# Kernel tuning notes

Measured on AMD Instinct MI355X. Metric: run time of the kernel, lower is better.

## Reference

```python
import jax, jax.numpy as jnp
import numpy as np

N, E, D, H = 100000, 200000, 384, 768
BN_EPS = 1e-5


def setup_inputs() -> dict:
    key = jax.random.key(0)
    ks = jax.random.split(key, 8)
    w = lambda k, sh: jax.random.normal(k, sh, jnp.float32) * 0.02
    return {
        "x": jax.random.normal(ks[0], (N, D), jnp.float32),
        "edge_attr": jax.random.normal(ks[1], (E, D), jnp.float32),
        "gamma": jnp.ones((D,), jnp.float32),
        "beta": jnp.zeros((D,), jnp.float32),
        "eps": jnp.zeros((), jnp.float32),          # GINE train_eps, init 0
        "W_edge": w(ks[2], (D, D)),
        "b_edge": jnp.zeros((D,), jnp.float32),
        "W1": w(ks[3], (D, H)),
        "b1": jnp.zeros((H,), jnp.float32),
        "W2": w(ks[4], (H, D)),
        "b2": jnp.zeros((D,), jnp.float32),
        "edge_index": jax.random.randint(ks[5], (2, E), 0, N, jnp.int32),
    }


def reference(x, edge_attr, gamma, beta, eps, W_edge, b_edge, W1, b1, W2, b2, edge_index):
    # BatchNorm1d over the node (batch) dimension, training statistics
    mu = jnp.mean(x, axis=0)
    var = jnp.var(x, axis=0)
    h = (x - mu) * jax.lax.rsqrt(var + BN_EPS) * gamma + beta  # [N, D]

    src, dst = edge_index[0], edge_index[1]  # j -> i (PyG source_to_target)
    # GINEConv message: relu(x_j + lin(edge_attr))
    msg = jax.nn.relu(h[src] + edge_attr @ W_edge + b_edge)     # [E, D]
    agg = jax.ops.segment_sum(msg, dst, num_segments=N)         # sum aggregation

    # nn((1+eps)*x_i + agg) where nn = Linear->GELU->Linear
    z = (1.0 + eps) * h + agg
    z = jax.nn.gelu(z @ W1 + b1, approximate=False) @ W2 + b2

    # residual + outer GELU activation (drop_path/dropout = identity at eval)
    return x + jax.nn.gelu(z, approximate=False)
```

## Files before the change

### kernel.cpp

```cpp
#include <hip/hip_runtime.h>
#include <hip/hip_bf16.h>

#define Df 384
#define Hf 768
#define SCAN_CH 4096

typedef __bf16 bf16x8 __attribute__((ext_vector_type(8)));
typedef float f32x4 __attribute__((ext_vector_type(4)));

struct __attribute__((aligned(4))) U12 { unsigned int x, y, z; };

__device__ inline unsigned short f2bf(float f) {
    __hip_bfloat16 h = __float2bfloat16(f);
    return __builtin_bit_cast(unsigned short, h);
}
__device__ inline float bf2f(unsigned short u) {
    unsigned int v = ((unsigned int)u) << 16;
    return __builtin_bit_cast(float, v);
}
__device__ inline float lobf(unsigned int v) { return bf2f((unsigned short)(v & 0xffff)); }
__device__ inline float hibf(unsigned int v) { return bf2f((unsigned short)(v >> 16)); }
__device__ inline unsigned int pk2(float a, float b) {
    return (unsigned int)f2bf(a) | ((unsigned int)f2bf(b) << 16);
}
__device__ inline float gelu_(float v) {
    return 0.5f * v * (1.0f + erff(v * 0.70710678118654752f));
}
__device__ inline void gload16(const void* g, void* l) {
    __builtin_amdgcn_global_load_lds(
        (const __attribute__((address_space(1))) unsigned int*)g,
        (__attribute__((address_space(3))) unsigned int*)l, 16, 0, 0);
}

__global__ void bn_stats(const float* __restrict__ x, float* __restrict__ stats, int N) {
    int t = threadIdx.x;
    int c4 = (t % 96) * 4;
    int rs = t / 96;
    float s0 = 0, s1 = 0, s2 = 0, s3 = 0, q0 = 0, q1 = 0, q2 = 0, q3 = 0;
    for (int r = blockIdx.x * 2 + rs; r < N; r += gridDim.x * 2) {
        float4 v = *(const float4*)(x + (size_t)r * Df + c4);
        s0 += v.x; s1 += v.y; s2 += v.z; s3 += v.w;
        q0 += v.x * v.x; q1 += v.y * v.y; q2 += v.z * v.z; q3 += v.w * v.w;
    }
    unsafeAtomicAdd(&stats[c4 + 0], s0);
    unsafeAtomicAdd(&stats[c4 + 1], s1);
    unsafeAtomicAdd(&stats[c4 + 2], s2);
    unsafeAtomicAdd(&stats[c4 + 3], s3);
    unsafeAtomicAdd(&stats[Df + c4 + 0], q0);
    unsafeAtomicAdd(&stats[Df + c4 + 1], q1);
    unsafeAtomicAdd(&stats[Df + c4 + 2], q2);
    unsafeAtomicAdd(&stats[Df + c4 + 3], q3);
}

__global__ void bn_finalize(const float* __restrict__ stats,
                            const float* __restrict__ gamma,
                            const float* __restrict__ beta,
                            float* __restrict__ coef, int N) {
    int c = threadIdx.x;
    float invN = 1.0f / (float)N;
    float mu = stats[c] * invN;
    float var = stats[Df + c] * invN - mu * mu;
    float rs = rsqrtf(var + 1e-5f);
    float a = gamma[c] * rs;
    coef[c] = a;
    coef[Df + c] = beta[c] - mu * a;
}

__global__ void h_kernel(const float* __restrict__ x, const float* __restrict__ coef,
                         unsigned short* __restrict__ hb, int tot8) {
    int i = blockIdx.x * 256 + threadIdx.x;
    if (i >= tot8) return;
    size_t base = (size_t)i * 8;
    int c = (int)(base % Df);
    float4 x0 = *(const float4*)(x + base);
    float4 x1 = *(const float4*)(x + base + 4);
    const float* a = coef + c;
    const float* b = coef + Df + c;
    uint4 o;
    o.x = pk2(x0.x * a[0] + b[0], x0.y * a[1] + b[1]);
    o.y = pk2(x0.z * a[2] + b[2], x0.w * a[3] + b[3]);
    o.z = pk2(x1.x * a[4] + b[4], x1.y * a[5] + b[5]);
    o.w = pk2(x1.z * a[6] + b[6], x1.w * a[7] + b[7]);
    *(uint4*)(hb + base) = o;
}

__global__ void wtrans3(const float* __restrict__ We, const float* __restrict__ W1,
                        const float* __restrict__ W2,
                        unsigned short* __restrict__ WeT, unsigned short* __restrict__ W1T,
                        unsigned short* __restrict__ W2T) {
    int idx = blockIdx.x * 256 + threadIdx.x;
    if (idx < Df * Df) {
        int k = idx / Df, n = idx % Df;
        WeT[n * Df + k] = f2bf(We[idx]);
    } else if (idx < Df * Df + Df * Hf) {
        int i = idx - Df * Df;
        int k = i / Hf, n = i % Hf;
        W1T[(size_t)n * Df + k] = f2bf(W1[i]);
    } else if (idx < Df * Df + 2 * Df * Hf) {
        int i = idx - (Df * Df + Df * Hf);
        int k = i / Df, n = i % Df;
        W2T[(size_t)n * Hf + k] = f2bf(W2[i]);
    }
}

__global__ void degree_k(const int* __restrict__ dst, int* __restrict__ deg, int E) {
    int e = blockIdx.x * 256 + threadIdx.x;
    if (e < E) atomicAdd(&deg[dst[e]], 1);
}

__global__ void scan1(const int* __restrict__ deg, int* __restrict__ off,
                      int* __restrict__ sums, int N) {
    __shared__ int ts[256];
    int t = threadIdx.x;
    int base = blockIdx.x * SCAN_CH + t * 16;
    int v[16];
    int s = 0;
    for (int j = 0; j < 16; j++) {
        int idx = base + j;
        int d = (idx < N) ? deg[idx] : 0;
        v[j] = s;
        s += d;
    }
    ts[t] = s;
    __syncthreads();
    for (int o = 1; o < 256; o <<= 1) {
        int add = (t >= o) ? ts[t - o] : 0;
        __syncthreads();
        ts[t] += add;
        __syncthreads();
    }
    int pre = t ? ts[t - 1] : 0;
    for (int j = 0; j < 16; j++) {
        int idx = base + j;
        if (idx < N) off[idx] = pre + v[j];
    }
    if (t == 255) sums[blockIdx.x] = ts[255];
}

__global__ void scan2(int* __restrict__ sums, int nb) {
    int acc = 0;
    for (int b = 0; b < nb; b++) { int v = sums[b]; sums[b] = acc; acc += v; }
    sums[nb] = acc;
}

__global__ void scan3(int* __restrict__ off, const int* __restrict__ sums, int N, int nb) {
    int idx = blockIdx.x * 256 + threadIdx.x;
    if (idx < N) off[idx] += sums[idx / SCAN_CH];
    else if (idx == N) off[N] = sums[nb];
}

__global__ void fill_k(const int* __restrict__ dst, const int* __restrict__ src,
                       int* __restrict__ cursor, int* __restrict__ srcp,
                       int* __restrict__ pose, int E) {
    int e = blockIdx.x * 256 + threadIdx.x;
    if (e >= E) return;
    int pos = atomicAdd(&cursor[dst[e]], 1);
    srcp[pos] = src[e];
    pose[e] = pos;
}

__global__ __launch_bounds__(256) void aggregate(
    const unsigned short* __restrict__ msgl, const unsigned short* __restrict__ hb,
    const int* __restrict__ off, const int* __restrict__ srcp,
    const float* __restrict__ epsp,
    unsigned short* __restrict__ zb, int N) {
    int lane = threadIdx.x & 63;
    int wid = threadIdx.x >> 6;
    int nwaves = gridDim.x * 4;
    float s1p = 1.0f + epsp[0];
    int loff = lane * 6;
    for (int i = blockIdx.x * 4 + wid; i < N; i += nwaves) {
        int o0 = off[i], o1 = off[i + 1];
        float a0 = 0, a1 = 0, a2 = 0, a3 = 0, a4 = 0, a5 = 0;
        for (int p = o0; p < o1; ++p) {
            int s = srcp[p];
            U12 mv = *(const U12*)(msgl + (size_t)p * Df + loff);
            U12 hv = *(const U12*)(hb + (size_t)s * Df + loff);
            a0 += fmaxf(lobf(mv.x) + lobf(hv.x), 0.f);
            a1 += fmaxf(hibf(mv.x) + hibf(hv.x), 0.f);
            a2 += fmaxf(lobf(mv.y) + lobf(hv.y), 0.f);
            a3 += fmaxf(hibf(mv.y) + hibf(hv.y), 0.f);
            a4 += fmaxf(lobf(mv.z) + lobf(hv.z), 0.f);
            a5 += fmaxf(hibf(mv.z) + hibf(hv.z), 0.f);
        }
        U12 hv = *(const U12*)(hb + (size_t)i * Df + loff);
        U12 o;
        o.x = pk2(s1p * lobf(hv.x) + a0, s1p * hibf(hv.x) + a1);
        o.y = pk2(s1p * lobf(hv.y) + a2, s1p * hibf(hv.y) + a3);
        o.z = pk2(s1p * lobf(hv.z) + a4, s1p * hibf(hv.z) + a5);
        *(U12*)(zb + (size_t)i * Df + loff) = o;
    }
}

template <int KTOT, int EPI>
__global__ __launch_bounds__(256, 3) void gemm_strip(
    const unsigned short* __restrict__ Ab, const unsigned short* __restrict__ Bt,
    const float* __restrict__ bias,
    unsigned short* __restrict__ outb, const float* __restrict__ xres,
    float* __restrict__ outf, int M, int ncols, int ldo) {
    constexpr int NKT = KTOT / 32;
    constexpr int NH = KTOT / 384;
    __shared__ __align__(16) unsigned short Bs[64 * 48 * 8];

    const int t = threadIdx.x;
    const int nwg = gridDim.x;
    const int orig = blockIdx.x;
    const int xcd = orig & 7;
    const int q = nwg >> 3, r = nwg & 7;
    const int wgid = (xcd < r ? xcd * (q + 1) : r * (q + 1) + (xcd - r) * q) + (orig >> 3);
    const int strip = wgid / ncols;
    const int cb = (wgid - strip * ncols) * 64;

    const int lane = t & 63;
    const int wid = t >> 6;
    const int fr = lane & 15;
    const int kg = lane >> 4;

    auto stageB = [&](int koff) {
#pragma unroll
        for (int s_ = 0; s_ < 12; s_++) {
            int u = s_ * 256 + t;
            int col = u / 48;
            int pos = u - col * 48;
            gload16(Bt + (size_t)(cb + col) * KTOT + koff + ((pos ^ (col & 7)) << 3),
                    &Bs[(s_ * 256 + wid * 64) * 8]);
        }
    };

    int ra0 = strip * 128 + wid * 32 + fr;      if (ra0 >= M) ra0 = M - 1;
    int ra1 = strip * 128 + wid * 32 + 16 + fr; if (ra1 >= M) ra1 = M - 1;
    const unsigned short* pA0 = Ab + (size_t)ra0 * KTOT + kg * 8;
    const unsigned short* pA1 = Ab + (size_t)ra1 * KTOT + kg * 8;

    f32x4 acc[2][4];
#pragma unroll
    for (int i = 0; i < 2; i++)
#pragma unroll
        for (int j = 0; j < 4; j++) acc[i][j] = (f32x4){0.f, 0.f, 0.f, 0.f};

    stageB(0);
    uint4 p0a = *(const uint4*)(pA0);       uint4 p0b = *(const uint4*)(pA1);
    uint4 p1a = *(const uint4*)(pA0 + 32);  uint4 p1b = *(const uint4*)(pA1 + 32);
    uint4 p2a = *(const uint4*)(pA0 + 64);  uint4 p2b = *(const uint4*)(pA1 + 64);
    asm volatile("s_waitcnt vmcnt(0)" ::: "memory");
    __builtin_amdgcn_s_barrier();

#define STEP(kt_, ktl_, pa_, pb_) do {                                          \
        bf16x8 bfv[4];                                                          \
        _Pragma("unroll")                                                       \
        for (int j_ = 0; j_ < 4; j_++) {                                        \
            const int cl_ = j_ * 16 + fr;                                       \
            const int unit_ = ((ktl_) * 4 + kg) ^ (cl_ & 7);                    \
            bfv[j_] = *(const bf16x8*)&Bs[(cl_ * 48 + unit_) * 8];              \
        }                                                                       \
        bf16x8 av0_ = __builtin_bit_cast(bf16x8, pa_);                          \
        bf16x8 av1_ = __builtin_bit_cast(bf16x8, pb_);                          \
        if ((kt_) + 3 < NKT) {                                                  \
            pa_ = *(const uint4*)(pA0 + ((kt_) + 3) * 32);                      \
            pb_ = *(const uint4*)(pA1 + ((kt_) + 3) * 32);                      \
        }                                                                       \
        _Pragma("unroll")                                                       \
        for (int j_ = 0; j_ < 4; j_++) {                                        \
            acc[0][j_] = __builtin_amdgcn_mfma_f32_16x16x32_bf16(av0_, bfv[j_], acc[0][j_], 0, 0, 0); \
            acc[1][j_] = __builtin_amdgcn_mfma_f32_16x16x32_bf16(av1_, bfv[j_], acc[1][j_], 0, 0, 0); \
        }                                                                       \
    } while (0)

#pragma unroll
    for (int h = 0; h < NH; h++) {
        if (h > 0) {
            __syncthreads();
            stageB(h * 384);
            asm volatile("s_waitcnt vmcnt(0)" ::: "memory");
            __builtin_amdgcn_s_barrier();
        }
#pragma unroll
        for (int kq = 0; kq < 4; kq++) {
            STEP(h * 12 + kq * 3 + 0, kq * 3 + 0, p0a, p0b);
            STEP(h * 12 + kq * 3 + 1, kq * 3 + 1, p1a, p1b);
            STEP(h * 12 + kq * 3 + 2, kq * 3 + 2, p2a, p2b);
        }
    }
#undef STEP

    float bv[4];
#pragma unroll
    for (int j = 0; j < 4; j++) bv[j] = bias[cb + j * 16 + fr];
    const int kg4 = kg * 4;
    const int rbase = strip * 128;

    if (EPI == 1) {
        __syncthreads();
        unsigned short* Ct = Bs;
#pragma unroll
        for (int i = 0; i < 2; i++) {
            const int rl = wid * 32 + i * 16 + kg4;
#pragma unroll
            for (int j = 0; j < 4; j++) {
#pragma unroll
                for (int rr = 0; rr < 4; rr++)
                    Ct[(rl + rr) * 72 + j * 16 + fr] = f2bf(gelu_(acc[i][j][rr] + bv[j]));
            }
        }
        __syncthreads();
#pragma unroll
        for (int s_ = 0; s_ < 4; s_++) {
            int u = s_ * 256 + t;
            int rl = u >> 3, seg = u & 7;
            int grow = rbase + rl;
            if (grow < M)
                *(uint4*)(outb + (size_t)grow * ldo + cb + seg * 8) =
                    *(const uint4*)&Ct[rl * 72 + seg * 8];
        }
    } else {
#pragma unroll
        for (int i = 0; i < 2; i++) {
            const int rb = rbase + wid * 32 + i * 16 + kg4;
#pragma unroll
            for (int rr = 0; rr < 4; rr++) {
                const int row = rb + rr;
                if (row < M) {
#pragma unroll
                    for (int j = 0; j < 4; j++) {
                        size_t o = (size_t)row * ldo + cb + j * 16 + fr;
                        outf[o] = xres[o] + gelu_(acc[i][j][rr] + bv[j]);
                    }
                }
            }
        }
    }
}

template <int EPI, bool ABF16>
__global__ __launch_bounds__(256) void gemm_fused(
    const void* __restrict__ Ap, const unsigned short* __restrict__ Bt,
    const float* __restrict__ bias, int M, int K, int ncols,
    const int* __restrict__ pose,
    unsigned short* __restrict__ outb,
    const float* __restrict__ xres, float* __restrict__ outf, int ldo) {
    __shared__ __align__(16) unsigned short As[2][128 * 32];
    __shared__ __align__(16) unsigned short Bs[2][128 * 32];
    const int t = threadIdx.x;
    const int nwg = gridDim.x;
    const int orig = blockIdx.x;
    const int xcd = orig & 7;
    const int q = nwg >> 3, r = nwg & 7;
    const int wgid = (xcd < r ? xcd * (q + 1) : r * (q + 1) + (xcd - r) * q) + (orig >> 3);
    const int pp = wgid / ncols;
    const int m0 = pp * 128;
    const int n0 = (wgid - pp * ncols) * 128;

    const int lane = t & 63;
    const int wid = t >> 6;
    const int wr = (wid >> 1) << 6;
    const int wc = (wid & 1) << 6;
    const int fr = lane & 15;
    const int kg = lane >> 4;
    const int crow = lane >> 2;
    const int cseg = lane & 3;
    const int sr = t >> 1;
    const int sh = (t & 1) << 4;

    f32x4 acc[4][4];
#pragma unroll
    for (int i = 0; i < 4; i++)
#pragma unroll
        for (int j = 0; j < 4; j++) acc[i][j] = (f32x4){0.f, 0.f, 0.f, 0.f};

    const bool arok = (m0 + sr) < M;
    const size_t arowoff = (size_t)(m0 + sr) * K;
    const int NT = K >> 5;

    auto stageB = [&](int buf, int k0) {
#pragma unroll
        for (int h = 0; h < 2; h++) {
            const int rbase = wid * 32 + h * 16;
            gload16(Bt + (size_t)(n0 + rbase + crow) * K + k0 + cseg * 8,
                    &Bs[buf][rbase * 32]);
        }
    };
    auto stageA16 = [&](int buf, int k0) {
        const unsigned short* Ab = (const unsigned short*)Ap;
#pragma unroll
        for (int h = 0; h < 2; h++) {
            const int rbase = wid * 32 + h * 16;
            if (m0 + rbase + crow < M)
                gload16(Ab + (size_t)(m0 + rbase + crow) * K + k0 + cseg * 8,
                        &As[buf][rbase * 32]);
        }
    };

    if (ABF16) {
        stageA16(0, 0);
    } else if (arok) {
        const float4* p = (const float4*)((const float*)Ap + arowoff + sh);
        float4 f0 = p[0], f1 = p[1], f2 = p[2], f3 = p[3];
        uint4 w0, w1;
        w0.x = pk2(f0.x, f0.y); w0.y = pk2(f0.z, f0.w);
        w0.z = pk2(f1.x, f1.y); w0.w = pk2(f1.z, f1.w);
        w1.x = pk2(f2.x, f2.y); w1.y = pk2(f2.z, f2.w);
        w1.z = pk2(f3.x, f3.y); w1.w = pk2(f3.z, f3.w);
        *(uint4*)&As[0][sr * 32 + sh] = w0;
        *(uint4*)&As[0][sr * 32 + sh + 8] = w1;
    }
    stageB(0, 0);
    __syncthreads();

    int cur = 0;
    for (int kt = 0; kt < NT; ++kt) {
        const int nxt = cur ^ 1;
        const bool more = (kt + 1) < NT;
        float4 f0, f1, f2, f3;
        if (more) {
            const int k0n = (kt + 1) * 32;
            if (ABF16) {
                stageA16(nxt, k0n);
            } else if (arok) {
                const float4* p = (const float4*)((const float*)Ap + arowoff + k0n + sh);
                f0 = p[0]; f1 = p[1]; f2 = p[2]; f3 = p[3];
            }
            stageB(nxt, k0n);
        }

        bf16x8 a[4], b[4];
#pragma unroll
        for (int i = 0; i < 4; i++) a[i] = *(const bf16x8*)&As[cur][(wr + i * 16 + fr) * 32 + kg * 8];
#pragma unroll
        for (int j = 0; j < 4; j++) b[j] = *(const bf16x8*)&Bs[cur][(wc + j * 16 + fr) * 32 + kg * 8];
#pragma unroll
        for (int i = 0; i < 4; i++)
#pragma unroll
            for (int j = 0; j < 4; j++)
                acc[i][j] = __builtin_amdgcn_mfma_f32_16x16x32_bf16(a[i], b[j], acc[i][j], 0, 0, 0);

        if (!ABF16 && more && arok) {
            uint4 w0, w1;
            w0.x = pk2(f0.x, f0.y); w0.y = pk2(f0.z, f0.w);
            w0.z = pk2(f1.x, f1.y); w0.w = pk2(f1.z, f1.w);
            w1.x = pk2(f2.x, f2.y); w1.y = pk2(f2.z, f2.w);
            w1.z = pk2(f3.x, f3.y); w1.w = pk2(f3.z, f3.w);
            *(uint4*)&As[nxt][sr * 32 + sh] = w0;
            *(uint4*)&As[nxt][sr * 32 + sh + 8] = w1;
        }
        __syncthreads();
        cur = nxt;
    }

    const int kg4 = kg * 4;
#pragma unroll
    for (int i = 0; i < 4; i++) {
        const int rb = m0 + wr + i * 16 + kg4;
#pragma unroll
        for (int j = 0; j < 4; j++) {
            const int c = n0 + wc + j * 16 + fr;
#pragma unroll
            for (int r = 0; r < 4; r++) {
                const int row = rb + r;
                if (row < M) {
                    float v = acc[i][j][r] + bias[c];
                    if (EPI == 2) {
                        size_t o = (size_t)row * ldo + c;
                        outf[o] = xres[o] + gelu_(v);
                    } else {
                        outb[(size_t)pose[row] * ldo + c] = f2bf(v);
                    }
                }
            }
        }
    }
}

extern "C" void kernel_launch(void* const* d_in, const int* in_sizes, int n_in,
                              void* d_out, int out_size, void* d_ws, size_t ws_size,
                              hipStream_t stream) {
    const float* x = (const float*)d_in[0];
    const float* ea = (const float*)d_in[1];
    const float* gamma = (const float*)d_in[2];
    const float* beta = (const float*)d_in[3];
    const float* epsp = (const float*)d_in[4];
    const float* W_edge = (const float*)d_in[5];
    const float* b_edge = (const float*)d_in[6];
    const float* W1 = (const float*)d_in[7];
    const float* b1 = (const float*)d_in[8];
    const float* W2 = (const float*)d_in[9];
    const float* b2 = (const float*)d_in[10];
    const int* eidx = (const int*)d_in[11];
    float* out = (float*)d_out;
    const int N = in_sizes[0] / Df;
    const int E = in_sizes[1] / Df;
    const int* esrc = eidx;
    const int* edst = eidx + E;

    char* w = (char*)d_ws;
    size_t off_ = 0;
    auto alloc = [&](size_t bytes) { char* p = w + off_; off_ += (bytes + 255) & ~(size_t)255; return p; };
    float* stats = (float*)alloc(2 * Df * sizeof(float));
    float* coef = (float*)alloc(2 * Df * sizeof(float));
    unsigned short* hb = (unsigned short*)alloc((size_t)N * Df * 2);
    unsigned short* zb = (unsigned short*)alloc((size_t)N * Df * 2);
    unsigned short* tb = (unsigned short*)alloc((size_t)N * Hf * 2);
    unsigned short* WeT = (unsigned short*)alloc((size_t)Df * Df * 2);
    unsigned short* W1T = (unsigned short*)alloc((size_t)Df * Hf * 2);
    unsigned short* W2T = (unsigned short*)alloc((size_t)Hf * Df * 2);
    int* deg = (int*)alloc((size_t)(N + 1) * 4);
    int* offs = (int*)alloc((size_t)(N + 1) * 4);
    int* srcp = (int*)alloc((size_t)E * 4);
    int* pose = (int*)alloc((size_t)E * 4);
    int* sums = (int*)alloc(64 * 4);
    size_t msgl_bytes = (size_t)E * Df * 2;
    unsigned short* msgl;
    if (off_ + msgl_bytes <= ws_size) msgl = (unsigned short*)alloc(msgl_bytes);
    else msgl = (unsigned short*)d_out;
    (void)n_in; (void)out_size;

    hipMemsetAsync(stats, 0, 2 * Df * sizeof(float), stream);
    hipMemsetAsync(deg, 0, (size_t)N * 4, stream);

    bn_stats<<<1024, 192, 0, stream>>>(x, stats, N);
    bn_finalize<<<1, Df, 0, stream>>>(stats, gamma, beta, coef, N);
    int tot8 = N * Df / 8;
    h_kernel<<<(tot8 + 255) / 256, 256, 0, stream>>>(x, coef, hb, tot8);

    wtrans3<<<(Df * Df + 2 * Df * Hf + 255) / 256, 256, 0, stream>>>(
        W_edge, W1, W2, WeT, W1T, W2T);

    int nb = (N + SCAN_CH - 1) / SCAN_CH;
    degree_k<<<(E + 255) / 256, 256, 0, stream>>>(edst, deg, E);
    scan1<<<nb, 256, 0, stream>>>(deg, offs, sums, N);
    scan2<<<1, 1, 0, stream>>>(sums, nb);
    scan3<<<(N + 256) / 256, 256, 0, stream>>>(offs, sums, N, nb);
    hipMemcpyAsync(deg, offs, (size_t)N * 4, hipMemcpyDeviceToDevice, stream);
    fill_k<<<(E + 255) / 256, 256, 0, stream>>>(edst, esrc, deg, srcp, pose, E);

    int ep = (E + 127) / 128;
    gemm_fused<3, false><<<dim3(ep * (Df / 128)), 256, 0, stream>>>(
        ea, WeT, b_edge, E, Df, Df / 128, pose, msgl, nullptr, nullptr, Df);

    aggregate<<<2048, 256, 0, stream>>>(msgl, hb, offs, srcp, epsp, zb, N);

    int strips = (N + 127) / 128;
    gemm_strip<Df, 1><<<dim3(strips * (Hf / 64)), 256, 0, stream>>>(
        zb, W1T, b1, tb, nullptr, nullptr, N, Hf / 64, Hf);

    gemm_strip<Hf, 2><<<dim3(strips * (Df / 64)), 256, 0, stream>>>(
        tb, W2T, b2, nullptr, x, out, N, Df / 64, Df);
}
```

Baseline: 1.029 ms.

## Rewrite edge GEMM with resident swizzled B tile and register-streamed fp32 A

Replaces the generic double-buffered 128x128 edge GEMM with a specialized kernel. It loads the full 64-column slice of W_edge (K=384) into swizzled LDS once per block, then streams fp32 edge_attr rows directly into registers with a three-deep prefetch and converts them to bf16 in registers, so A never passes through LDS and the per-k-step barriers go away. Output is staged through LDS so the scatter to the pose-permuted rows uses 16-byte row-contiguous stores instead of scattered 2-byte stores. The cost is six column blocks per row strip, each rereading the same A rows, and more register pressure under the launch bound of 3.

```diff
diff --git a/kernel.cpp b/kernel.cpp
--- a/kernel.cpp
+++ b/kernel.cpp
@@ -331,142 +331,123 @@
     }
 }
 
-template <int EPI, bool ABF16>
-__global__ __launch_bounds__(256) void gemm_fused(
-    const void* __restrict__ Ap, const unsigned short* __restrict__ Bt,
-    const float* __restrict__ bias, int M, int K, int ncols,
-    const int* __restrict__ pose,
-    unsigned short* __restrict__ outb,
-    const float* __restrict__ xres, float* __restrict__ outf, int ldo) {
-    __shared__ __align__(16) unsigned short As[2][128 * 32];
-    __shared__ __align__(16) unsigned short Bs[2][128 * 32];
+__global__ __launch_bounds__(256, 3) void gemm_edge(
+    const float* __restrict__ Af, const unsigned short* __restrict__ Bt,
+    const float* __restrict__ bias, const int* __restrict__ pose,
+    unsigned short* __restrict__ outb, int M) {
+    __shared__ __align__(16) unsigned short Bs[64 * 48 * 8];
+
     const int t = threadIdx.x;
     const int nwg = gridDim.x;
     const int orig = blockIdx.x;
     const int xcd = orig & 7;
     const int q = nwg >> 3, r = nwg & 7;
     const int wgid = (xcd < r ? xcd * (q + 1) : r * (q + 1) + (xcd - r) * q) + (orig >> 3);
-    const int pp = wgid / ncols;
-    const int m0 = pp * 128;
-    const int n0 = (wgid - pp * ncols) * 128;
+    const int strip = wgid / 6;
+    const int cb = (wgid - strip * 6) * 64;
 
     const int lane = t & 63;
     const int wid = t >> 6;
-    const int wr = (wid >> 1) << 6;
-    const int wc = (wid & 1) << 6;
     const int fr = lane & 15;
     const int kg = lane >> 4;
-    const int crow = lane >> 2;
-    const int cseg = lane & 3;
-    const int sr = t >> 1;
-    const int sh = (t & 1) << 4;
-
-    f32x4 acc[4][4];
-#pragma unroll
-    for (int i = 0; i < 4; i++)
+
+#pragma unroll
+    for (int s_ = 0; s_ < 12; s_++) {
+        int u = s_ * 256 + t;
+        int col = u / 48;
+        int pos = u - col * 48;
+        gload16(Bt + (size_t)(cb + col) * Df + ((pos ^ (col & 7)) << 3),
+                &Bs[(s_ * 256 + wid * 64) * 8]);
+    }
+
+    int ra0 = strip * 128 + wid * 32 + fr;      if (ra0 >= M) ra0 = M - 1;
+    int ra1 = strip * 128 + wid * 32 + 16 + fr; if (ra1 >= M) ra1 = M - 1;
+    const float* pA0 = Af + (size_t)ra0 * Df + kg * 8;
+    const float* pA1 = Af + (size_t)ra1 * Df + kg * 8;
+
+    f32x4 acc[2][4];
+#pragma unroll
+    for (int i = 0; i < 2; i++)
 #pragma unroll
         for (int j = 0; j < 4; j++) acc[i][j] = (f32x4){0.f, 0.f, 0.f, 0.f};
 
-    const bool arok = (m0 + sr) < M;
-    const size_t arowoff = (size_t)(m0 + sr) * K;
-    const int NT = K >> 5;
-
-    auto stageB = [&](int buf, int k0) {
-#pragma unroll
-        for (int h = 0; h < 2; h++) {
-            const int rbase = wid * 32 + h * 16;
-            gload16(Bt + (size_t)(n0 + rbase + crow) * K + k0 + cseg * 8,
-                    &Bs[buf][rbase * 32]);
-        }
-    };
-    auto stageA16 = [&](int buf, int k0) {
-        const unsigned short* Ab = (const unsigned short*)Ap;
-#pragma unroll
-        for (int h = 0; h < 2; h++) {
-            const int rbase = wid * 32 + h * 16;
-            if (m0 + rbase + crow < M)
-                gload16(Ab + (size_t)(m0 + rbase + crow) * K + k0 + cseg * 8,
-                        &As[buf][rbase * 32]);
-        }
-    };
-
-    if (ABF16) {
-        stageA16(0, 0);
-    } else if (arok) {
-        const float4* p = (const float4*)((const float*)Ap + arowoff + sh);
-        float4 f0 = p[0], f1 = p[1], f2 = p[2], f3 = p[3];
-        uint4 w0, w1;
-        w0.x = pk2(f0.x, f0.y); w0.y = pk2(f0.z, f0.w);
-        w0.z = pk2(f1.x, f1.y); w0.w = pk2(f1.z, f1.w);
-        w1.x = pk2(f2.x, f2.y); w1.y = pk2(f2.z, f2.w);
-        w1.z = pk2(f3.x, f3.y); w1.w = pk2(f3.z, f3.w);
-        *(uint4*)&As[0][sr * 32 + sh] = w0;
-        *(uint4*)&As[0][sr * 32 + sh + 8] = w1;
-    }
-    stageB(0, 0);
+    uint4 p0al = *(const uint4*)(pA0);       uint4 p0ah = *(const uint4*)(pA0 + 4);
+    uint4 p0bl = *(const uint4*)(pA1);       uint4 p0bh = *(const uint4*)(pA1 + 4);
+    uint4 p1al = *(const uint4*)(pA0 + 32);  uint4 p1ah = *(const uint4*)(pA0 + 36);
+    uint4 p1bl = *(const uint4*)(pA1 + 32);  uint4 p1bh = *(const uint4*)(pA1 + 36);
+    uint4 p2al = *(const uint4*)(pA0 + 64);  uint4 p2ah = *(const uint4*)(pA0 + 68);
+    uint4 p2bl = *(const uint4*)(pA1 + 64);  uint4 p2bh = *(const uint4*)(pA1 + 68);
+    asm volatile("s_waitcnt vmcnt(0)" ::: "memory");
+    __builtin_amdgcn_s_barrier();
+
+#define ESTEP(kt_, pal_, pah_, pbl_, pbh_) do {                                 \
+        bf16x8 bfv[4];                                                          \
+        _Pragma("unroll")                                                       \
+        for (int j_ = 0; j_ < 4; j_++) {                                        \
+            const int cl_ = j_ * 16 + fr;                                       \
+            const int unit_ = ((kt_) * 4 + kg) ^ (cl_ & 7);                     \
+            bfv[j_] = *(const bf16x8*)&Bs[(cl_ * 48 + unit_) * 8];              \
+        }                                                                       \
+        float4 xa0_ = __builtin_bit_cast(float4, pal_);                         \
+        float4 xa1_ = __builtin_bit_cast(float4, pah_);                         \
+        uint4 ua_;                                                              \
+        ua_.x = pk2(xa0_.x, xa0_.y); ua_.y = pk2(xa0_.z, xa0_.w);               \
+        ua_.z = pk2(xa1_.x, xa1_.y); ua_.w = pk2(xa1_.z, xa1_.w);               \
+        bf16x8 av0_ = __builtin_bit_cast(bf16x8, ua_);                          \
+        float4 xb0_ = __builtin_bit_cast(float4, pbl_);                         \
+        float4 xb1_ = __builtin_bit_cast(float4, pbh_);                         \
+        uint4 ub_;                                                              \
+        ub_.x = pk2(xb0_.x, xb0_.y); ub_.y = pk2(xb0_.z, xb0_.w);               \
+        ub_.z = pk2(xb1_.x, xb1_.y); ub_.w = pk2(xb1_.z, xb1_.w);               \
+        bf16x8 av1_ = __builtin_bit_cast(bf16x8, ub_);                          \
+        if ((kt_) + 3 < 12) {                                                   \
+            pal_ = *(const uint4*)(pA0 + ((kt_) + 3) * 32);                     \
+            pah_ = *(const uint4*)(pA0 + ((kt_) + 3) * 32 + 4);                 \
+            pbl_ = *(const uint4*)(pA1 + ((kt_) + 3) * 32);                     \
+            pbh_ = *(const uint4*)(pA1 + ((kt_) + 3) * 32 + 4);                 \
+        }                                                                       \
+        _Pragma("unroll")                                                       \
+        for (int j_ = 0; j_ < 4; j_++) {                                        \
+            acc[0][j_] = __builtin_amdgcn_mfma_f32_16x16x32_bf16(av0_, bfv[j_], acc[0][j_], 0, 0, 0); \
+            acc[1][j_] = __builtin_amdgcn_mfma_f32_16x16x32_bf16(av1_, bfv[j_], acc[1][j_], 0, 0, 0); \
+        }                                                                       \
+    } while (0)
+
+#pragma unroll
+    for (int kq = 0; kq < 4; kq++) {
+        ESTEP(kq * 3 + 0, p0al, p0ah, p0bl, p0bh);
+        ESTEP(kq * 3 + 1, p1al, p1ah, p1bl, p1bh);
+        ESTEP(kq * 3 + 2, p2al, p2ah, p2bl, p2bh);
+    }
+#undef ESTEP
+
+    float bv[4];
+#pragma unroll
+    for (int j = 0; j < 4; j++) bv[j] = bias[cb + j * 16 + fr];
+    const int kg4 = kg * 4;
+    const int rbase = strip * 128;
+
     __syncthreads();
-
-    int cur = 0;
-    for (int kt = 0; kt < NT; ++kt) {
-        const int nxt = cur ^ 1;
-        const bool more = (kt + 1) < NT;
-        float4 f0, f1, f2, f3;
-        if (more) {
-            const int k0n = (kt + 1) * 32;
-            if (ABF16) {
-                stageA16(nxt, k0n);
-            } else if (arok) {
-                const float4* p = (const float4*)((const float*)Ap + arowoff + k0n + sh);
-                f0 = p[0]; f1 = p[1]; f2 = p[2]; f3 = p[3];
-            }
-            stageB(nxt, k0n);
-        }
-
-        bf16x8 a[4], b[4];
-#pragma unroll
-        for (int i = 0; i < 4; i++) a[i] = *(const bf16x8*)&As[cur][(wr + i * 16 + fr) * 32 + kg * 8];
-#pragma unroll
-        for (int j = 0; j < 4; j++) b[j] = *(const bf16x8*)&Bs[cur][(wc + j * 16 + fr) * 32 + kg * 8];
-#pragma unroll
-        for (int i = 0; i < 4; i++)
-#pragma unroll
-            for (int j = 0; j < 4; j++)
-                acc[i][j] = __builtin_amdgcn_mfma_f32_16x16x32_bf16(a[i], b[j], acc[i][j], 0, 0, 0);
-
-        if (!ABF16 && more && arok) {
-            uint4 w0, w1;
-            w0.x = pk2(f0.x, f0.y); w0.y = pk2(f0.z, f0.w);
-            w0.z = pk2(f1.x, f1.y); w0.w = pk2(f1.z, f1.w);
-            w1.x = pk2(f2.x, f2.y); w1.y = pk2(f2.z, f2.w);
-            w1.z = pk2(f3.x, f3.y); w1.w = pk2(f3.z, f3.w);
-            *(uint4*)&As[nxt][sr * 32 + sh] = w0;
-            *(uint4*)&As[nxt][sr * 32 + sh + 8] = w1;
-        }
-        __syncthreads();
-        cur = nxt;
-    }
-
-    const int kg4 = kg * 4;
-#pragma unroll
-    for (int i = 0; i < 4; i++) {
-        const int rb = m0 + wr + i * 16 + kg4;
+    unsigned short* Ct = Bs;
+#pragma unroll
+    for (int i = 0; i < 2; i++) {
+        const int rl = wid * 32 + i * 16 + kg4;
 #pragma unroll
         for (int j = 0; j < 4; j++) {
-            const int c = n0 + wc + j * 16 + fr;
-#pragma unroll
-            for (int r = 0; r < 4; r++) {
-                const int row = rb + r;
-                if (row < M) {
-                    float v = acc[i][j][r] + bias[c];
-                    if (EPI == 2) {
-                        size_t o = (size_t)row * ldo + c;
-                        outf[o] = xres[o] + gelu_(v);
-                    } else {
-                        outb[(size_t)pose[row] * ldo + c] = f2bf(v);
-                    }
-                }
-            }
-        }
+#pragma unroll
+            for (int rr = 0; rr < 4; rr++)
+                Ct[(rl + rr) * 72 + j * 16 + fr] = f2bf(acc[i][j][rr] + bv[j]);
+        }
+    }
+    __syncthreads();
+#pragma unroll
+    for (int s_ = 0; s_ < 4; s_++) {
+        int u = s_ * 256 + t;
+        int rl = u >> 3, seg = u & 7;
+        int grow = rbase + rl;
+        if (grow < M)
+            *(uint4*)(outb + (size_t)pose[grow] * Df + cb + seg * 8) =
+                *(const uint4*)&Ct[rl * 72 + seg * 8];
     }
 }
 
@@ -532,9 +513,8 @@
     hipMemcpyAsync(deg, offs, (size_t)N * 4, hipMemcpyDeviceToDevice, stream);
     fill_k<<<(E + 255) / 256, 256, 0, stream>>>(edst, esrc, deg, srcp, pose, E);
 
-    int ep = (E + 127) / 128;
-    gemm_fused<3, false><<<dim3(ep * (Df / 128)), 256, 0, stream>>>(
-        ea, WeT, b_edge, E, Df, Df / 128, pose, msgl, nullptr, nullptr, Df);
+    int estrips = (E + 127) / 128;
+    gemm_edge<<<dim3(estrips * 6), 256, 0, stream>>>(ea, WeT, b_edge, pose, msgl, E);
 
     aggregate<<<2048, 256, 0, stream>>>(msgl, hb, offs, srcp, epsp, zb, N);
 
```

Measured after the change: 1.059 ms. +2.9%, slower.
